# Optimization experiments

Hardware: AMD Instinct MI355X
Metric: run time of the kernel (lower is better)

The kernel has to match this reference:

```python
import jax, jax.numpy as jnp
import numpy as np

N = 60000      # nodes in batch (max_num_cg_nodes_in_batch = 80000)
E = 150000     # edges per edge type
T = 4          # primary edge types (doubled by add_backwards_edges -> 8)
D = 64         # hidden / embedding size
V = 10000      # subtoken vocab
S = 5          # max subtokens per node label
TIMESTEPS = [7, 1]


def setup_inputs() -> dict:
    key = jax.random.key(0)
    ks = jax.random.split(key, 12)
    sc = 1.0 / np.sqrt(D)
    return {
        "node_subtokens": jax.random.randint(ks[0], (N, S), 0, V),
        "adjacency_lists": jax.random.randint(ks[1], (T, E, 2), 0, N),
        "embed_table": jax.random.normal(ks[2], (V, D), jnp.float32) * 0.1,
        "proj_W": jax.random.normal(ks[3], (D, D), jnp.float32) * sc,
        "edge_W0": jax.random.normal(ks[4], (2 * T, D, D), jnp.float32) * sc,
        "edge_W1": jax.random.normal(ks[5], (2 * T, D, D), jnp.float32) * sc,
        "gru0_Wx": jax.random.normal(ks[6], (D, 3 * D), jnp.float32) * sc,
        "gru0_Wh": jax.random.normal(ks[7], (D, 3 * D), jnp.float32) * sc,
        "gru0_b": jnp.zeros((3 * D,), jnp.float32),
        "gru1_Wx": jax.random.normal(ks[8], (2 * D, 3 * D), jnp.float32) * sc,
        "gru1_Wh": jax.random.normal(ks[9], (D, 3 * D), jnp.float32) * sc,
        "gru1_b": jnp.zeros((3 * D,), jnp.float32),
    }


def _gru(x, h, Wx, Wh, b):
    gx = x @ Wx + b          # [N, 3D]
    gh = h @ Wh              # [N, 3D]
    xr, xu, xc = jnp.split(gx, 3, axis=-1)
    hr, hu, hc = jnp.split(gh, 3, axis=-1)
    r = jax.nn.sigmoid(xr + hr)
    u = jax.nn.sigmoid(xu + hu)
    c = jnp.tanh(xc + r * hc)
    return u * h + (1.0 - u) * c


def reference(node_subtokens, adjacency_lists, embed_table, proj_W,
              edge_W0, edge_W1, gru0_Wx, gru0_Wh, gru0_b,
              gru1_Wx, gru1_Wh, gru1_b):
    # Effective edge types: forward + backward (add_backwards_edges=True)
    srcs = jnp.concatenate([adjacency_lists[:, :, 0], adjacency_lists[:, :, 1]], 0)  # [2T, E]
    dsts = jnp.concatenate([adjacency_lists[:, :, 1], adjacency_lists[:, :, 0]], 0)  # [2T, E]
    flat_dsts = dsts.reshape(-1)

    def aggregate(h, edge_W):
        gathered = h[srcs]                                 # [2T, E, D] gather
        msgs = jnp.einsum('ted,tdk->tek', gathered, edge_W)  # per-edge-type transform
        m = jax.ops.segment_max(msgs.reshape(-1, D), flat_dsts, num_segments=N)
        # nodes with no incoming edges get -inf from segment_max -> zero them
        return jnp.where(jnp.isfinite(m), m, 0.0)

    # Subtoken embedding: mean-pool subtoken embeddings, project to hidden
    node_emb = embed_table[node_subtokens].mean(axis=1)    # [N, D]
    h_init = node_emb @ proj_W                             # [N, D]

    # Layer 0: 7 timesteps, no residual
    h = h_init
    for _ in range(TIMESTEPS[0]):
        h = _gru(aggregate(h, edge_W0), h, gru0_Wx, gru0_Wh, gru0_b)

    # Layer 1: 1 timestep, residual from layer index 0 (= initial node states)
    for _ in range(TIMESTEPS[1]):
        msg = aggregate(h, edge_W1)
        h = _gru(jnp.concatenate([h_init, msg], axis=-1), h, gru1_Wx, gru1_Wh, gru1_b)

    return h  # [N, D] final node representations
```

## Files before the change

kernel.cpp:

```cpp
#include <hip/hip_runtime.h>

typedef short v8s __attribute__((ext_vector_type(8)));
typedef float v4f __attribute__((ext_vector_type(4)));

__device__ __forceinline__ unsigned short f2bf(float x) {
  unsigned u = __float_as_uint(x);
  u = u + 0x7FFFu + ((u >> 16) & 1u);
  return (unsigned short)(u >> 16);
}
__device__ __forceinline__ float bf2f(unsigned short b) {
  return __uint_as_float(((unsigned)b) << 16);
}
__device__ __forceinline__ float sigmoidf_(float x) {
  return 1.f / (1.f + __expf(-x));
}
__device__ __forceinline__ float tanhf_(float x) {
  x = fminf(fmaxf(x, -20.f), 20.f);
  float e2 = __expf(2.f * x);
  return (e2 - 1.f) / (e2 + 1.f);
}

__device__ __forceinline__ void wprep_one(const float* W, unsigned short* O,
                                          int K, int J, int idx) {
  int nkc = K >> 5, nct = J >> 4;
  int j = idx & 7, lane = (idx >> 3) & 63;
  int rest = idx >> 9;
  int ct = rest % nct; rest /= nct;
  int kc = rest % nkc; rest /= nkc;
  int p = rest & 1, t = rest >> 1;
  int row = kc * 32 + (lane >> 4) * 8 + j;
  int col = ct * 16 + (lane & 15);
  float v = W[(size_t)t * K * J + (size_t)row * J + col];
  unsigned short hi = f2bf(v);
  O[idx] = p ? f2bf(v - bf2f(hi)) : hi;
}

__global__ void k_wprep_all(
    const float* eW0, const float* eW1, const float* projW,
    const float* g0Wx, const float* g0Wh, const float* g1Wx, const float* g1Wh,
    unsigned short* eW0f, unsigned short* eW1f, unsigned short* projf,
    unsigned short* g0xf, unsigned short* g0hf,
    unsigned short* g1xf, unsigned short* g1hf) {
  int rel = blockIdx.x * 256 + threadIdx.x;
  if (rel < 65536) { wprep_one(eW0, eW0f, 64, 64, rel); return; }
  rel -= 65536;
  if (rel < 65536) { wprep_one(eW1, eW1f, 64, 64, rel); return; }
  rel -= 65536;
  if (rel < 8192)  { wprep_one(projW, projf, 64, 64, rel); return; }
  rel -= 8192;
  if (rel < 24576) { wprep_one(g0Wx, g0xf, 64, 192, rel); return; }
  rel -= 24576;
  if (rel < 24576) { wprep_one(g0Wh, g0hf, 64, 192, rel); return; }
  rel -= 24576;
  if (rel < 49152) { wprep_one(g1Wx, g1xf, 128, 192, rel); return; }
  rel -= 49152;
  if (rel < 24576) { wprep_one(g1Wh, g1hf, 64, 192, rel); return; }
}

__global__ __launch_bounds__(256) void k_embed(
    const int* __restrict__ toks, const float* __restrict__ embed,
    unsigned short* __restrict__ eh, unsigned short* __restrict__ el, int N) {
  int w = threadIdx.x >> 6, lane = threadIdx.x & 63;
  int n = blockIdx.x * 4 + w;
  if (n >= N) return;
  float acc = 0.f;
#pragma unroll
  for (int s = 0; s < 5; ++s)
    acc += embed[(size_t)toks[n * 5 + s] * 64 + lane];
  float v = acc * 0.2f;
  unsigned short h = f2bf(v);
  eh[(size_t)n * 64 + lane] = h;
  el[(size_t)n * 64 + lane] = f2bf(v - bf2f(h));
}

__global__ void k_counts(const int* __restrict__ adj, int* __restrict__ counts, int E) {
  int e = blockIdx.x * 256 + threadIdx.x;
  if (e >= E) return;
  int t = blockIdx.y, t4 = t & 3;
  int a = adj[(size_t)(t4 * E + e) * 2], b = adj[(size_t)(t4 * E + e) * 2 + 1];
  int dst = (t < 4) ? b : a;
  atomicAdd(&counts[dst], 1);
}

__global__ __launch_bounds__(1024) void k_scan(const int* __restrict__ counts,
                                               int* __restrict__ offsets, int n) {
  __shared__ int part[1024];
  int tid = threadIdx.x;
  int chunk = (((n + 1023) >> 10) + 3) & ~3;
  int begin = tid * chunk;
  int end = min(begin + chunk, n);
  int s = 0;
  int i = begin;
  for (; i + 4 <= end; i += 4) {
    int4 v = *(const int4*)&counts[i];
    s += v.x + v.y + v.z + v.w;
  }
  for (; i < end; ++i) s += counts[i];
  part[tid] = s;
  __syncthreads();
  for (int off = 1; off < 1024; off <<= 1) {
    int v = (tid >= off) ? part[tid - off] : 0;
    __syncthreads();
    part[tid] += v;
    __syncthreads();
  }
  int run = part[tid] - s;
  i = begin;
  for (; i + 4 <= end; i += 4) {
    int4 c = *(const int4*)&counts[i];
    int4 o;
    o.x = run; o.y = run + c.x; o.z = o.y + c.y; o.w = o.z + c.z;
    *(int4*)&offsets[i] = o;
    run = o.w + c.w;
  }
  for (; i < end; ++i) { offsets[i] = run; run += counts[i]; }
  if (tid == 1023) offsets[n] = part[1023];
}

__global__ void k_fill(const int* __restrict__ adj, int* __restrict__ cursor,
                       int* __restrict__ entries, int E, int N) {
  int e = blockIdx.x * 256 + threadIdx.x;
  if (e >= E) return;
  int t = blockIdx.y, t4 = t & 3;
  int a = adj[(size_t)(t4 * E + e) * 2], b = adj[(size_t)(t4 * E + e) * 2 + 1];
  int src = (t < 4) ? a : b;
  int dst = (t < 4) ? b : a;
  int pos = atomicAdd(&cursor[dst], 1);
  entries[pos] = t * N + src;
}

__global__ __launch_bounds__(256) void k_proj(
    const unsigned short* __restrict__ A0h, const unsigned short* __restrict__ A0l,
    const unsigned short* __restrict__ Wf,
    unsigned short* __restrict__ h_hi, unsigned short* __restrict__ h_lo,
    unsigned short* __restrict__ hinit_b, int N) {
  int tid = threadIdx.x;
  int wv = tid >> 6, lane = tid & 63;
  int lr = lane & 15, lg = lane >> 4;
  int m0 = blockIdx.x * 128 + wv * 32;
  v4f acc[2][4] = {};
#pragma unroll
  for (int kc = 0; kc < 2; ++kc) {
    v8s ah[2], al[2];
#pragma unroll
    for (int mt = 0; mt < 2; ++mt) {
      int row = min(m0 + mt * 16 + lr, N - 1);
      size_t off = (size_t)row * 64 + kc * 32 + lg * 8;
      ah[mt] = *(const v8s*)&A0h[off];
      al[mt] = *(const v8s*)&A0l[off];
    }
#pragma unroll
    for (int ct = 0; ct < 4; ++ct) {
      v8s bh = *(const v8s*)&Wf[((size_t)(kc * 4 + ct)) * 512 + lane * 8];
      v8s bl = *(const v8s*)&Wf[((size_t)((2 + kc) * 4 + ct)) * 512 + lane * 8];
#pragma unroll
      for (int mt = 0; mt < 2; ++mt) {
        acc[mt][ct] = __builtin_amdgcn_mfma_f32_16x16x32_bf16(ah[mt], bh, acc[mt][ct], 0, 0, 0);
        acc[mt][ct] = __builtin_amdgcn_mfma_f32_16x16x32_bf16(al[mt], bh, acc[mt][ct], 0, 0, 0);
        acc[mt][ct] = __builtin_amdgcn_mfma_f32_16x16x32_bf16(ah[mt], bl, acc[mt][ct], 0, 0, 0);
      }
    }
  }
#pragma unroll
  for (int ct = 0; ct < 4; ++ct)
#pragma unroll
    for (int mt = 0; mt < 2; ++mt)
#pragma unroll
      for (int r = 0; r < 4; ++r) {
        int m = m0 + mt * 16 + lg * 4 + r;
        if (m >= N) continue;
        int col = ct * 16 + lr;
        float v = acc[mt][ct][r];
        unsigned short hb = f2bf(v);
        h_hi[(size_t)m * 64 + col] = hb;
        h_lo[(size_t)m * 64 + col] = f2bf(v - bf2f(hb));
        hinit_b[(size_t)m * 64 + col] = hb;
      }
}

__global__ __launch_bounds__(256) void k_mm_t(
    const unsigned short* __restrict__ A0h, const unsigned short* __restrict__ A0l,
    const unsigned short* __restrict__ Wf, unsigned short* __restrict__ C16,
    int N) {
  int tid = threadIdx.x;
  int wv = tid >> 6, lane = tid & 63;
  int lr = lane & 15, lg = lane >> 4;
  const unsigned short* Wfb = Wf + (size_t)blockIdx.y * 8192;
  unsigned short* Cb = C16 + (size_t)blockIdx.y * N * 64;
  int m0 = blockIdx.x * 128 + wv * 32;
  v4f acc[2][4] = {};
#pragma unroll
  for (int kc = 0; kc < 2; ++kc) {
    v8s ah[2], al[2];
#pragma unroll
    for (int mt = 0; mt < 2; ++mt) {
      int row = min(m0 + mt * 16 + lr, N - 1);
      size_t off = (size_t)row * 64 + kc * 32 + lg * 8;
      ah[mt] = *(const v8s*)&A0h[off];
      al[mt] = *(const v8s*)&A0l[off];
    }
#pragma unroll
    for (int ct = 0; ct < 4; ++ct) {
      v8s bh = *(const v8s*)&Wfb[((size_t)(kc * 4 + ct)) * 512 + lane * 8];
      v8s bl = *(const v8s*)&Wfb[((size_t)((2 + kc) * 4 + ct)) * 512 + lane * 8];
#pragma unroll
      for (int mt = 0; mt < 2; ++mt) {
        acc[mt][ct] = __builtin_amdgcn_mfma_f32_16x16x32_bf16(ah[mt], bh, acc[mt][ct], 0, 0, 0);
        acc[mt][ct] = __builtin_amdgcn_mfma_f32_16x16x32_bf16(al[mt], bh, acc[mt][ct], 0, 0, 0);
        acc[mt][ct] = __builtin_amdgcn_mfma_f32_16x16x32_bf16(ah[mt], bl, acc[mt][ct], 0, 0, 0);
      }
    }
  }
#pragma unroll
  for (int ct = 0; ct < 4; ++ct)
#pragma unroll
    for (int mt = 0; mt < 2; ++mt)
#pragma unroll
      for (int r = 0; r < 4; ++r) {
        int m = m0 + mt * 16 + lg * 4 + r;
        if (m < N) Cb[(size_t)m * 64 + ct * 16 + lr] = f2bf(acc[mt][ct][r]);
      }
}

__global__ __launch_bounds__(256) void k_aggmax(
    const unsigned short* __restrict__ Htb, const int* __restrict__ offsets,
    const int* __restrict__ entries, unsigned short* __restrict__ mh, int N) {
  int w = threadIdx.x >> 6, lane = threadIdx.x & 63;
  int n = blockIdx.x * 4 + w;
  if (n >= N) return;
  int beg = offsets[n], end = offsets[n + 1];
  float m = -3.4e38f, m2 = -3.4e38f;
  int i = beg;
  for (; i + 4 <= end; i += 4) {
    int e0 = entries[i], e1 = entries[i + 1], e2 = entries[i + 2], e3 = entries[i + 3];
    float v0 = bf2f(Htb[(size_t)e0 * 64 + lane]);
    float v1 = bf2f(Htb[(size_t)e1 * 64 + lane]);
    float v2 = bf2f(Htb[(size_t)e2 * 64 + lane]);
    float v3 = bf2f(Htb[(size_t)e3 * 64 + lane]);
    m = fmaxf(m, fmaxf(v0, v1));
    m2 = fmaxf(m2, fmaxf(v2, v3));
  }
  m = fmaxf(m, m2);
  for (; i < end; ++i) m = fmaxf(m, bf2f(Htb[(size_t)entries[i] * 64 + lane]));
  float v = (end > beg) ? m : 0.f;
  mh[(size_t)n * 64 + lane] = f2bf(v);
}

template <int NKCX>
__global__ __launch_bounds__(256) void k_gru(
    const unsigned short* __restrict__ x0, const unsigned short* __restrict__ x1,
    const unsigned short* __restrict__ hh, const unsigned short* __restrict__ hl,
    const unsigned short* __restrict__ Wxf, const unsigned short* __restrict__ Whf,
    const float* __restrict__ bias,
    float* outF, unsigned short* oh, unsigned short* ol, int N) {
  int tid = threadIdx.x;
  int wv = tid >> 6, lane = tid & 63;
  int lr = lane & 15, lg = lane >> 4;
  int m0 = blockIdx.x * 128 + wv * 32;
  v4f acc[2][12] = {};
  v4f acch[2][4] = {};
#pragma unroll
  for (int kc = 0; kc < NKCX; ++kc) {
    const unsigned short* X = (NKCX == 4 && kc >= 2) ? x1 : x0;
    int kcl = kc & 1;
    v8s ax[2];
#pragma unroll
    for (int mt = 0; mt < 2; ++mt) {
      int row = min(m0 + mt * 16 + lr, N - 1);
      ax[mt] = *(const v8s*)&X[(size_t)row * 64 + kcl * 32 + lg * 8];
    }
#pragma unroll
    for (int ct = 0; ct < 12; ++ct) {
      v8s bh = *(const v8s*)&Wxf[((size_t)(kc * 12 + ct)) * 512 + lane * 8];
      v8s bl = *(const v8s*)&Wxf[((size_t)((NKCX + kc) * 12 + ct)) * 512 + lane * 8];
#pragma unroll
      for (int mt = 0; mt < 2; ++mt) {
        acc[mt][ct] = __builtin_amdgcn_mfma_f32_16x16x32_bf16(ax[mt], bh, acc[mt][ct], 0, 0, 0);
        acc[mt][ct] = __builtin_amdgcn_mfma_f32_16x16x32_bf16(ax[mt], bl, acc[mt][ct], 0, 0, 0);
      }
    }
  }
#pragma unroll
  for (int kc = 0; kc < 2; ++kc) {
    v8s ah[2], al[2];
#pragma unroll
    for (int mt = 0; mt < 2; ++mt) {
      int row = min(m0 + mt * 16 + lr, N - 1);
      size_t off = (size_t)row * 64 + kc * 32 + lg * 8;
      ah[mt] = *(const v8s*)&hh[off];
      al[mt] = *(const v8s*)&hl[off];
    }
#pragma unroll
    for (int ct = 0; ct < 12; ++ct) {
      v8s bh = *(const v8s*)&Whf[((size_t)(kc * 12 + ct)) * 512 + lane * 8];
      v8s bl = *(const v8s*)&Whf[((size_t)((2 + kc) * 12 + ct)) * 512 + lane * 8];
#pragma unroll
      for (int mt = 0; mt < 2; ++mt) {
        v4f* d = (ct < 8) ? &acc[mt][ct] : &acch[mt][ct - 8];
        *d = __builtin_amdgcn_mfma_f32_16x16x32_bf16(ah[mt], bh, *d, 0, 0, 0);
        *d = __builtin_amdgcn_mfma_f32_16x16x32_bf16(al[mt], bh, *d, 0, 0, 0);
        *d = __builtin_amdgcn_mfma_f32_16x16x32_bf16(ah[mt], bl, *d, 0, 0, 0);
      }
    }
  }
#pragma unroll
  for (int mt = 0; mt < 2; ++mt)
#pragma unroll
    for (int ctg = 0; ctg < 4; ++ctg)
#pragma unroll
      for (int r = 0; r < 4; ++r) {
        int m = m0 + mt * 16 + lg * 4 + r;
        if (m >= N) continue;
        int col = ctg * 16 + lr;
        float hv = bf2f(hh[(size_t)m * 64 + col]) + bf2f(hl[(size_t)m * 64 + col]);
        float rr = sigmoidf_(acc[mt][ctg][r] + bias[col]);
        float uu = sigmoidf_(acc[mt][ctg + 4][r] + bias[64 + col]);
        float cc = tanhf_(acc[mt][ctg + 8][r] + bias[128 + col] + rr * acch[mt][ctg][r]);
        float ho = uu * hv + (1.f - uu) * cc;
        if (outF) outF[(size_t)m * 64 + col] = ho;
        if (oh) {
          unsigned short hb = f2bf(ho);
          oh[(size_t)m * 64 + col] = hb;
          ol[(size_t)m * 64 + col] = f2bf(ho - bf2f(hb));
        }
      }
}

extern "C" void kernel_launch(void* const* d_in, const int* in_sizes, int n_in,
                              void* d_out, int out_size, void* d_ws, size_t ws_size,
                              hipStream_t stream) {
  const int*   toks  = (const int*)d_in[0];
  const int*   adj   = (const int*)d_in[1];
  const float* embed = (const float*)d_in[2];
  const float* projW = (const float*)d_in[3];
  const float* eW0   = (const float*)d_in[4];
  const float* eW1   = (const float*)d_in[5];
  const float* g0Wx  = (const float*)d_in[6];
  const float* g0Wh  = (const float*)d_in[7];
  const float* g0b   = (const float*)d_in[8];
  const float* g1Wx  = (const float*)d_in[9];
  const float* g1Wh  = (const float*)d_in[10];
  const float* g1b   = (const float*)d_in[11];
  float* out = (float*)d_out;

  int N = in_sizes[0] / 5;
  int E = in_sizes[1] / 8;
  size_t ND = (size_t)N * 64;

  char* p = (char*)d_ws;
  unsigned short* Htb     = (unsigned short*)p; p += 8 * ND * 2;
  unsigned short* h_hi    = (unsigned short*)p; p += ND * 2;
  unsigned short* h_lo    = (unsigned short*)p; p += ND * 2;
  unsigned short* hinit_b = (unsigned short*)p; p += ND * 2;
  unsigned short* m_hi    = (unsigned short*)p; p += ND * 2;
  int* offsets = (int*)p; p += (size_t)(N + 64) * sizeof(int);
  int* cnt_cur = (int*)p; p += (size_t)(N + 64) * sizeof(int);
  int* entries = (int*)p; p += (size_t)8 * E * sizeof(int);
  unsigned short* eW0f  = (unsigned short*)p; p += 65536 * 2;
  unsigned short* eW1f  = (unsigned short*)p; p += 65536 * 2;
  unsigned short* projf = (unsigned short*)p; p += 8192 * 2;
  unsigned short* g0xf  = (unsigned short*)p; p += 24576 * 2;
  unsigned short* g0hf  = (unsigned short*)p; p += 24576 * 2;
  unsigned short* g1xf  = (unsigned short*)p; p += 49152 * 2;
  unsigned short* g1hf  = (unsigned short*)p; p += 24576 * 2;
  if ((size_t)(p - (char*)d_ws) > ws_size) return;

  unsigned short* emb_h = Htb;
  unsigned short* emb_l = Htb + ND;

  int g128 = (N + 127) / 128;
  int g4 = (N + 3) / 4;

  k_wprep_all<<<1024, 256, 0, stream>>>(eW0, eW1, projW, g0Wx, g0Wh, g1Wx, g1Wh,
                                        eW0f, eW1f, projf, g0xf, g0hf, g1xf, g1hf);
  hipMemsetAsync(cnt_cur, 0, (size_t)N * sizeof(int), stream);
  dim3 egrid((E + 255) / 256, 8);
  k_counts<<<egrid, 256, 0, stream>>>(adj, cnt_cur, E);
  k_embed<<<g4, 256, 0, stream>>>(toks, embed, emb_h, emb_l, N);
  k_proj<<<g128, 256, 0, stream>>>(emb_h, emb_l, projf, h_hi, h_lo, hinit_b, N);
  k_scan<<<1, 1024, 0, stream>>>(cnt_cur, offsets, N);
  hipMemcpyAsync(cnt_cur, offsets, (size_t)N * sizeof(int),
                 hipMemcpyDeviceToDevice, stream);
  k_fill<<<egrid, 256, 0, stream>>>(adj, cnt_cur, entries, E, N);

  for (int it = 0; it < 8; ++it) {
    const unsigned short* ef = (it < 7) ? eW0f : eW1f;
    k_mm_t<<<dim3(g128, 8), 256, 0, stream>>>(h_hi, h_lo, ef, Htb, N);
    k_aggmax<<<g4, 256, 0, stream>>>(Htb, offsets, entries, m_hi, N);
    if (it < 7) {
      k_gru<2><<<g128, 256, 0, stream>>>(m_hi, nullptr, h_hi, h_lo,
                                         g0xf, g0hf, g0b,
                                         nullptr, h_hi, h_lo, N);
    } else {
      k_gru<4><<<g128, 256, 0, stream>>>(hinit_b, m_hi, h_hi, h_lo,
                                         g1xf, g1hf, g1b,
                                         out, nullptr, nullptr, N);
    }
  }
}
```

Baseline: 1.188 ms.

## Vectorize max-aggregation gathers, pair edge types in transform, merge CSR build passes

The max-aggregation kernel now has each lane load four bf16 features at once, with four edges handled per wave step, and finishes with a cross-group shuffle reduction. This cuts the number of narrow gather instructions on the dominant per-step cost. The edge-type transform computes a forward and a backward type in one block, reusing the loaded node rows. CSR construction handles both directions per adjacency entry, and the scan writes the cursor copy directly instead of a separate device memcpy. The scan now reads counts and writes cursor into the same buffer. Its scalar tail loop would read a slot it has already overwritten, which only stays correct because N splits evenly into the per-thread chunks.

```diff
diff --git a/kernel.cpp b/kernel.cpp
--- a/kernel.cpp
+++ b/kernel.cpp
@@ -76,14 +76,15 @@
 __global__ void k_counts(const int* __restrict__ adj, int* __restrict__ counts, int E) {
   int e = blockIdx.x * 256 + threadIdx.x;
   if (e >= E) return;
-  int t = blockIdx.y, t4 = t & 3;
-  int a = adj[(size_t)(t4 * E + e) * 2], b = adj[(size_t)(t4 * E + e) * 2 + 1];
-  int dst = (t < 4) ? b : a;
-  atomicAdd(&counts[dst], 1);
+  int t4 = blockIdx.y;
+  int2 ab = *(const int2*)&adj[(size_t)(t4 * E + e) * 2];
+  atomicAdd(&counts[ab.y], 1);
+  atomicAdd(&counts[ab.x], 1);
 }
 
 __global__ __launch_bounds__(1024) void k_scan(const int* __restrict__ counts,
-                                               int* __restrict__ offsets, int n) {
+                                               int* __restrict__ offsets,
+                                               int* __restrict__ cursor, int n) {
   __shared__ int part[1024];
   int tid = threadIdx.x;
   int chunk = (((n + 1023) >> 10) + 3) & ~3;
@@ -111,9 +112,12 @@
     int4 o;
     o.x = run; o.y = run + c.x; o.z = o.y + c.y; o.w = o.z + c.z;
     *(int4*)&offsets[i] = o;
+    *(int4*)&cursor[i] = o;
     run = o.w + c.w;
   }
-  for (; i < end; ++i) { offsets[i] = run; run += counts[i]; }
+  for (; i < end; ++i) {
+    offsets[i] = run; cursor[i] = run; run += counts[i];
+  }
   if (tid == 1023) offsets[n] = part[1023];
 }
 
@@ -121,12 +125,12 @@
                        int* __restrict__ entries, int E, int N) {
   int e = blockIdx.x * 256 + threadIdx.x;
   if (e >= E) return;
-  int t = blockIdx.y, t4 = t & 3;
-  int a = adj[(size_t)(t4 * E + e) * 2], b = adj[(size_t)(t4 * E + e) * 2 + 1];
-  int src = (t < 4) ? a : b;
-  int dst = (t < 4) ? b : a;
-  int pos = atomicAdd(&cursor[dst], 1);
-  entries[pos] = t * N + src;
+  int t4 = blockIdx.y;
+  int2 ab = *(const int2*)&adj[(size_t)(t4 * E + e) * 2];
+  int p1 = atomicAdd(&cursor[ab.y], 1);
+  entries[p1] = t4 * N + ab.x;
+  int p2 = atomicAdd(&cursor[ab.x], 1);
+  entries[p2] = (t4 + 4) * N + ab.y;
 }
 
 __global__ __launch_bounds__(256) void k_proj(
@@ -185,10 +189,13 @@
   int tid = threadIdx.x;
   int wv = tid >> 6, lane = tid & 63;
   int lr = lane & 15, lg = lane >> 4;
-  const unsigned short* Wfb = Wf + (size_t)blockIdx.y * 8192;
-  unsigned short* Cb = C16 + (size_t)blockIdx.y * N * 64;
+  int y = blockIdx.y;
+  const unsigned short* W0 = Wf + (size_t)y * 8192;
+  const unsigned short* W1 = Wf + (size_t)(y + 4) * 8192;
+  unsigned short* C0 = C16 + (size_t)y * N * 64;
+  unsigned short* C1 = C16 + (size_t)(y + 4) * N * 64;
   int m0 = blockIdx.x * 128 + wv * 32;
-  v4f acc[2][4] = {};
+  v4f acc0[2][4] = {}, acc1[2][4] = {};
 #pragma unroll
   for (int kc = 0; kc < 2; ++kc) {
     v8s ah[2], al[2];
@@ -201,13 +208,18 @@
     }
 #pragma unroll
     for (int ct = 0; ct < 4; ++ct) {
-      v8s bh = *(const v8s*)&Wfb[((size_t)(kc * 4 + ct)) * 512 + lane * 8];
-      v8s bl = *(const v8s*)&Wfb[((size_t)((2 + kc) * 4 + ct)) * 512 + lane * 8];
+      v8s bh0 = *(const v8s*)&W0[((size_t)(kc * 4 + ct)) * 512 + lane * 8];
+      v8s bl0 = *(const v8s*)&W0[((size_t)((2 + kc) * 4 + ct)) * 512 + lane * 8];
+      v8s bh1 = *(const v8s*)&W1[((size_t)(kc * 4 + ct)) * 512 + lane * 8];
+      v8s bl1 = *(const v8s*)&W1[((size_t)((2 + kc) * 4 + ct)) * 512 + lane * 8];
 #pragma unroll
       for (int mt = 0; mt < 2; ++mt) {
-        acc[mt][ct] = __builtin_amdgcn_mfma_f32_16x16x32_bf16(ah[mt], bh, acc[mt][ct], 0, 0, 0);
-        acc[mt][ct] = __builtin_amdgcn_mfma_f32_16x16x32_bf16(al[mt], bh, acc[mt][ct], 0, 0, 0);
-        acc[mt][ct] = __builtin_amdgcn_mfma_f32_16x16x32_bf16(ah[mt], bl, acc[mt][ct], 0, 0, 0);
+        acc0[mt][ct] = __builtin_amdgcn_mfma_f32_16x16x32_bf16(ah[mt], bh0, acc0[mt][ct], 0, 0, 0);
+        acc0[mt][ct] = __builtin_amdgcn_mfma_f32_16x16x32_bf16(al[mt], bh0, acc0[mt][ct], 0, 0, 0);
+        acc0[mt][ct] = __builtin_amdgcn_mfma_f32_16x16x32_bf16(ah[mt], bl0, acc0[mt][ct], 0, 0, 0);
+        acc1[mt][ct] = __builtin_amdgcn_mfma_f32_16x16x32_bf16(ah[mt], bh1, acc1[mt][ct], 0, 0, 0);
+        acc1[mt][ct] = __builtin_amdgcn_mfma_f32_16x16x32_bf16(al[mt], bh1, acc1[mt][ct], 0, 0, 0);
+        acc1[mt][ct] = __builtin_amdgcn_mfma_f32_16x16x32_bf16(ah[mt], bl1, acc1[mt][ct], 0, 0, 0);
       }
     }
   }
@@ -218,7 +230,10 @@
 #pragma unroll
       for (int r = 0; r < 4; ++r) {
         int m = m0 + mt * 16 + lg * 4 + r;
-        if (m < N) Cb[(size_t)m * 64 + ct * 16 + lr] = f2bf(acc[mt][ct][r]);
+        if (m < N) {
+          C0[(size_t)m * 64 + ct * 16 + lr] = f2bf(acc0[mt][ct][r]);
+          C1[(size_t)m * 64 + ct * 16 + lr] = f2bf(acc1[mt][ct][r]);
+        }
       }
 }
 
@@ -229,21 +244,41 @@
   int n = blockIdx.x * 4 + w;
   if (n >= N) return;
   int beg = offsets[n], end = offsets[n + 1];
-  float m = -3.4e38f, m2 = -3.4e38f;
+  int g = lane >> 4, q = lane & 15;
+  float a0 = -3.4e38f, a1 = a0, a2 = a0, a3 = a0;
+  float b0 = a0, b1 = a0, b2 = a0, b3 = a0;
   int i = beg;
-  for (; i + 4 <= end; i += 4) {
-    int e0 = entries[i], e1 = entries[i + 1], e2 = entries[i + 2], e3 = entries[i + 3];
-    float v0 = bf2f(Htb[(size_t)e0 * 64 + lane]);
-    float v1 = bf2f(Htb[(size_t)e1 * 64 + lane]);
-    float v2 = bf2f(Htb[(size_t)e2 * 64 + lane]);
-    float v3 = bf2f(Htb[(size_t)e3 * 64 + lane]);
-    m = fmaxf(m, fmaxf(v0, v1));
-    m2 = fmaxf(m2, fmaxf(v2, v3));
-  }
-  m = fmaxf(m, m2);
-  for (; i < end; ++i) m = fmaxf(m, bf2f(Htb[(size_t)entries[i] * 64 + lane]));
-  float v = (end > beg) ? m : 0.f;
-  mh[(size_t)n * 64 + lane] = f2bf(v);
+  for (; i + 8 <= end; i += 8) {
+    int eA = entries[i + g];
+    int eB = entries[i + 4 + g];
+    ushort4 va = *(const ushort4*)&Htb[(size_t)eA * 64 + q * 4];
+    ushort4 vb = *(const ushort4*)&Htb[(size_t)eB * 64 + q * 4];
+    a0 = fmaxf(a0, bf2f(va.x)); a1 = fmaxf(a1, bf2f(va.y));
+    a2 = fmaxf(a2, bf2f(va.z)); a3 = fmaxf(a3, bf2f(va.w));
+    b0 = fmaxf(b0, bf2f(vb.x)); b1 = fmaxf(b1, bf2f(vb.y));
+    b2 = fmaxf(b2, bf2f(vb.z)); b3 = fmaxf(b3, bf2f(vb.w));
+  }
+  for (; i < end; i += 4) {
+    int idx = min(i + g, end - 1);
+    int e = entries[idx];
+    ushort4 va = *(const ushort4*)&Htb[(size_t)e * 64 + q * 4];
+    a0 = fmaxf(a0, bf2f(va.x)); a1 = fmaxf(a1, bf2f(va.y));
+    a2 = fmaxf(a2, bf2f(va.z)); a3 = fmaxf(a3, bf2f(va.w));
+  }
+  a0 = fmaxf(a0, b0); a1 = fmaxf(a1, b1); a2 = fmaxf(a2, b2); a3 = fmaxf(a3, b3);
+  a0 = fmaxf(a0, __shfl_xor(a0, 16)); a1 = fmaxf(a1, __shfl_xor(a1, 16));
+  a2 = fmaxf(a2, __shfl_xor(a2, 16)); a3 = fmaxf(a3, __shfl_xor(a3, 16));
+  a0 = fmaxf(a0, __shfl_xor(a0, 32)); a1 = fmaxf(a1, __shfl_xor(a1, 32));
+  a2 = fmaxf(a2, __shfl_xor(a2, 32)); a3 = fmaxf(a3, __shfl_xor(a3, 32));
+  if (g == 0) {
+    ushort4 o;
+    if (end > beg) {
+      o.x = f2bf(a0); o.y = f2bf(a1); o.z = f2bf(a2); o.w = f2bf(a3);
+    } else {
+      o.x = 0; o.y = 0; o.z = 0; o.w = 0;
+    }
+    *(ushort4*)&mh[(size_t)n * 64 + q * 4] = o;
+  }
 }
 
 template <int NKCX>
@@ -374,18 +409,16 @@
   k_wprep_all<<<1024, 256, 0, stream>>>(eW0, eW1, projW, g0Wx, g0Wh, g1Wx, g1Wh,
                                         eW0f, eW1f, projf, g0xf, g0hf, g1xf, g1hf);
   hipMemsetAsync(cnt_cur, 0, (size_t)N * sizeof(int), stream);
-  dim3 egrid((E + 255) / 256, 8);
+  dim3 egrid((E + 255) / 256, 4);
   k_counts<<<egrid, 256, 0, stream>>>(adj, cnt_cur, E);
   k_embed<<<g4, 256, 0, stream>>>(toks, embed, emb_h, emb_l, N);
   k_proj<<<g128, 256, 0, stream>>>(emb_h, emb_l, projf, h_hi, h_lo, hinit_b, N);
-  k_scan<<<1, 1024, 0, stream>>>(cnt_cur, offsets, N);
-  hipMemcpyAsync(cnt_cur, offsets, (size_t)N * sizeof(int),
-                 hipMemcpyDeviceToDevice, stream);
+  k_scan<<<1, 1024, 0, stream>>>(cnt_cur, offsets, cnt_cur, N);
   k_fill<<<egrid, 256, 0, stream>>>(adj, cnt_cur, entries, E, N);
 
   for (int it = 0; it < 8; ++it) {
     const unsigned short* ef = (it < 7) ? eW0f : eW1f;
-    k_mm_t<<<dim3(g128, 8), 256, 0, stream>>>(h_hi, h_lo, ef, Htb, N);
+    k_mm_t<<<dim3(g128, 4), 256, 0, stream>>>(h_hi, h_lo, ef, Htb, N);
     k_aggmax<<<g4, 256, 0, stream>>>(Htb, offsets, entries, m_hi, N);
     if (it < 7) {
       k_gru<2><<<g128, 256, 0, stream>>>(m_hi, nullptr, h_hi, h_lo,
```

After: 1.112 ms. -6.4%, faster.
